# Performance work log

Hardware: AMD Instinct MI355X
Metric: run time of the kernel (lower is better)

## Reference

```python
import jax, jax.numpy as jnp
import numpy as np

R, NU, NM, E = 5, 100000, 100000, 1000000
IN, MSG, OUT, BAS = 64, 80, 64, 4
MPR = MSG // R  # per-rating message units (stack agg)


def setup_inputs() -> dict:
    key = jax.random.key(0)
    ks = jax.random.split(key, 12)
    return {
        "ufeat": jax.random.normal(ks[0], (NU, IN), jnp.float32),
        "ifeat": jax.random.normal(ks[1], (NM, IN), jnp.float32),
        "cj_user": jax.random.uniform(ks[2], (NU, 1), jnp.float32) + 0.1,
        "ci_user": jax.random.uniform(ks[3], (NU, 1), jnp.float32) + 0.1,
        "cj_movie": jax.random.uniform(ks[4], (NM, 1), jnp.float32) + 0.1,
        "ci_movie": jax.random.uniform(ks[5], (NM, 1), jnp.float32) + 0.1,
        "edge_user": jax.random.randint(ks[6], (R, E), 0, NU, jnp.int32),
        "edge_movie": jax.random.randint(ks[7], (R, E), 0, NM, jnp.int32),
        "att": jax.random.normal(ks[8], (R, BAS), jnp.float32),
        "basis": jax.random.normal(ks[9], (BAS, IN, MPR), jnp.float32),
        "fc_w": jax.random.normal(ks[10], (OUT, MSG), jnp.float32) / np.sqrt(MSG),
        "fc_b": jnp.zeros((OUT,), jnp.float32),
    }


def _agg(feat, src, dst, cj, ci, n_dst):
    # gather src features scaled by cj, scatter-sum to dst, scale by ci
    m = feat[src] * cj[src]                                 # [E, MPR]
    out = jax.ops.segment_sum(m, dst, num_segments=n_dst)   # [n_dst, MPR]
    return out * ci


def reference(ufeat, ifeat, cj_user, ci_user, cj_movie, ci_movie,
              edge_user, edge_movie, att, basis, fc_w, fc_b):
    # per-rating weights from basis decomposition
    W = jnp.einsum('rb,bio->rio', att, basis)       # [R, IN, MPR]
    fu = jnp.einsum('ni,rio->rno', ufeat, W)        # [R, NU, MPR]
    fi = jnp.einsum('ni,rio->rno', ifeat, W)        # [R, NM, MPR]
    agg = jax.vmap(_agg, in_axes=(0, 0, 0, None, None, None))
    # forward edges: user -> movie; reverse edges: movie -> user
    m_out = agg(fu, edge_user, edge_movie, cj_user, ci_movie, NM)  # [R, NM, MPR]
    u_out = agg(fi, edge_movie, edge_user, cj_movie, ci_user, NU)  # [R, NU, MPR]
    # 'stack' cross-type aggregation, flattened over ratings
    u = jnp.transpose(u_out, (1, 0, 2)).reshape(NU, MSG)
    m = jnp.transpose(m_out, (1, 0, 2)).reshape(NM, MSG)
    u = jax.nn.relu(u) @ fc_w.T + fc_b   # shared ufc == ifc
    m = jax.nn.relu(m) @ fc_w.T + fc_b
    return u, m
```

## Files before the change

kernel.cpp:

```cpp
#include <hip/hip_runtime.h>
#include <cstdint>
#include <cstddef>

constexpr int kR   = 5;
constexpr int kNU  = 100000;
constexpr int kNM  = 100000;
constexpr int kE   = 1000000;
constexpr int kIN  = 64;
constexpr int kMSG = 80;
constexpr int kOUT = 64;
constexpr int kBAS = 4;
constexpr int kMPR = 16;

constexpr int kN        = 100000;
constexpr unsigned kEdges   = (unsigned)kR * (unsigned)kE;
constexpr unsigned kTotRecs = 2u * kEdges;

constexpr int kBD        = 80;
constexpr int kNB        = kN / kBD;
constexpr unsigned kCap  = 5632;
constexpr int kChunkE    = 8192;
constexpr int kDirBlocks = (int)((kEdges + kChunkE - 1) / kChunkE);
constexpr int kMsgBlocks = (kN + 255) / 256;

constexpr float kScale    = 64.0f;
constexpr float kInvScale = 1.0f / 64.0f;

constexpr int kStride = 17;
constexpr int kAccWords = kBD * kR * kStride;

__global__ __launch_bounds__(256) void gcmc_init(
    uint32_t* __restrict__ cursor, const float* __restrict__ fc_w,
    float* __restrict__ Wq)
{
    const int t = blockIdx.x * 256 + threadIdx.x;
    if (t < 2 * kNB) cursor[t] = (uint32_t)t * kCap;
    if (t < 20 * kOUT * 4) {
        const int q  = t & 3;
        const int o  = (t >> 2) & 63;
        const int j4 = t >> 8;
        Wq[t] = fc_w[o * kMSG + j4 * 4 + q];
    }
}

__device__ __forceinline__ uint32_t pack2i16(float x, float y) {
    const int ix = (int)rintf(fminf(fmaxf(x, -32760.f), 32760.f));
    const int iy = (int)rintf(fminf(fmaxf(y, -32760.f), 32760.f));
    return (uint32_t)(ix & 0xFFFF) | ((uint32_t)(iy & 0xFFFF) << 16);
}

__global__ __launch_bounds__(256) void gcmc_msg(
    const float* __restrict__ ufeat, const float* __restrict__ ifeat,
    const float* __restrict__ cj_user, const float* __restrict__ cj_movie,
    const float* __restrict__ att,  const float* __restrict__ basis,
    short* __restrict__ ms)
{
    __shared__ float Wl[kR * kIN * kMPR];
    const int tid  = threadIdx.x;
    const int side = blockIdx.x >= kMsgBlocks;
    const int blk  = blockIdx.x - side * kMsgBlocks;
    const float* feat = side ? ifeat : ufeat;
    const float* cj   = side ? cj_movie : cj_user;
    uint2* mout = reinterpret_cast<uint2*>(ms + (side ? (size_t)kR * kN * kMPR : 0));

    for (int idx = tid; idx < kR * kIN * kMPR; idx += 256) {
        const int r   = idx >> 10;
        const int rem = idx & 1023;
        const int i   = rem >> 4;
        const int k   = rem & 15;
        float s = 0.f;
#pragma unroll
        for (int b = 0; b < kBAS; ++b)
            s += att[r * kBAS + b] * basis[(b * kIN + i) * kMPR + k];
        Wl[idx] = s;
    }
    __syncthreads();

    const int node = blk * 256 + tid;
    if (node >= kN) return;

    float f[kIN];
    const float4* fp = reinterpret_cast<const float4*>(feat + (size_t)node * kIN);
#pragma unroll
    for (int i = 0; i < kIN / 4; ++i) {
        float4 v = fp[i];
        f[4 * i + 0] = v.x; f[4 * i + 1] = v.y;
        f[4 * i + 2] = v.z; f[4 * i + 3] = v.w;
    }
    const float c = cj[node] * kScale;
    const float4* W4 = reinterpret_cast<const float4*>(Wl);

    for (int r = 0; r < kR; ++r) {
#pragma unroll
        for (int kg = 0; kg < kMPR / 4; ++kg) {
            float4 a = make_float4(0.f, 0.f, 0.f, 0.f);
#pragma unroll
            for (int i = 0; i < kIN; ++i) {
                float4 w = W4[(r * kIN + i) * (kMPR / 4) + kg];
                a.x += f[i] * w.x; a.y += f[i] * w.y;
                a.z += f[i] * w.z; a.w += f[i] * w.w;
            }
            const uint32_t plane = (uint32_t)(r * kN + node);
            mout[plane * 4u + kg] =
                make_uint2(pack2i16(a.x * c, a.y * c), pack2i16(a.z * c, a.w * c));
        }
    }
}

__global__ __launch_bounds__(512) void gcmc_partition(
    const int* __restrict__ dst0, const int* __restrict__ src0,
    const int* __restrict__ dst1, const int* __restrict__ src1,
    uint32_t* __restrict__ cursor, uint32_t* __restrict__ bucket_recs)
{
    __shared__ uint32_t hist[kNB];
    __shared__ uint32_t excl[kNB];
    __shared__ uint32_t gbase[kNB];
    __shared__ uint32_t scanT[512];
    __shared__ uint32_t stage[kChunkE];
    __shared__ uint16_t sbkt[kChunkE];
    const int tid = threadIdx.x;
    const int dir = blockIdx.x >= kDirBlocks;
    const int blk = blockIdx.x - dir * kDirBlocks;
    const int* dsts = dir ? dst1 : dst0;
    const int* srcs = dir ? src1 : src0;

    for (int i = tid; i < kNB; i += 512) hist[i] = 0;
    __syncthreads();

    const unsigned base = (unsigned)blk * kChunkE;
    uint32_t rec[16], bk[16], rk[16];
#pragma unroll
    for (int j = 0; j < 16; ++j) {
        const unsigned idx = base + j * 512u + tid;
        if (idx < kEdges) {
            const unsigned d = (unsigned)dsts[idx];
            const unsigned s = (unsigned)srcs[idx];
            const unsigned r = idx / (unsigned)kE;
            const unsigned b = d / (unsigned)kBD;
            const unsigned dl = d - b * (unsigned)kBD;
            rec[j] = (r * (unsigned)kN + s) | ((dl * (unsigned)kR + r) << 19);
            bk[j]  = b;
            rk[j]  = atomicAdd(&hist[b], 1u);
        } else bk[j] = 0xFFFFFFFFu;
    }
    __syncthreads();

    uint32_t loc[3]; uint32_t s2 = 0;
#pragma unroll
    for (int q = 0; q < 3; ++q) {
        const int b = tid * 3 + q;
        loc[q] = (b < kNB) ? hist[b] : 0u;
        s2 += loc[q];
    }
    scanT[tid] = s2; __syncthreads();
    for (int off = 1; off < 512; off <<= 1) {
        const uint32_t v = (tid >= off) ? scanT[tid - off] : 0u;
        __syncthreads();
        scanT[tid] += v;
        __syncthreads();
    }
    const uint32_t total = scanT[511];
    uint32_t run = scanT[tid] - s2;
#pragma unroll
    for (int q = 0; q < 3; ++q) {
        const int b = tid * 3 + q;
        if (b < kNB) {
            excl[b]  = run;
            gbase[b] = loc[q] ? atomicAdd(&cursor[dir * kNB + b], loc[q]) : 0u;
        }
        run += loc[q];
    }
    __syncthreads();

#pragma unroll
    for (int j = 0; j < 16; ++j) {
        if (bk[j] != 0xFFFFFFFFu) {
            const uint32_t p = excl[bk[j]] + rk[j];
            stage[p] = rec[j];
            sbkt[p]  = (uint16_t)bk[j];
        }
    }
    __syncthreads();

    for (unsigned p = tid; p < total; p += 512) {
        const uint32_t b = sbkt[p];
        bucket_recs[gbase[b] + (p - excl[b])] = stage[p];
    }
}

__global__ __launch_bounds__(256, 5) void gcmc_accum_fc(
    const short* __restrict__ ms,
    const uint32_t* __restrict__ bucket_recs,
    const uint32_t* __restrict__ cursor,
    const float* __restrict__ ci_user, const float* __restrict__ ci_movie,
    const float* __restrict__ Wq, const float* __restrict__ fc_b,
    float* __restrict__ out_u, float* __restrict__ out_m)
{
    __shared__ int accI[kAccWords];
    const int tid = threadIdx.x;
    const int db  = blockIdx.x;
    const int dir = db >= kNB;
    const int bl  = db - dir * kNB;

    for (int i = tid; i < kAccWords; i += 256) accI[i] = 0;
    __syncthreads();

    const uint32_t gb0 = (uint32_t)db * kCap;
    const uint32_t n   = cursor[db] - gb0;
    const uint32_t* rp = bucket_recs + gb0;
    const int l = tid & 3;
    const int g = tid >> 2;
    const uint2* pb = reinterpret_cast<const uint2*>(
        ms + (dir ? (size_t)kR * kN * kMPR : 0));

#define RRR(IDX) { const uint32_t rc = rp[(IDX)];                          \
                   const uint2 v = pb[(rc & 0x7FFFFu) * 4u + (unsigned)l];  \
                   const int w = (int)(rc >> 19) * kStride + (l << 2);      \
                   atomicAdd(&accI[w + 0], (int)(short)v.x);                \
                   atomicAdd(&accI[w + 1], ((int)v.x) >> 16);               \
                   atomicAdd(&accI[w + 2], (int)(short)v.y);                \
                   atomicAdd(&accI[w + 3], ((int)v.y) >> 16); }

    uint32_t i = (uint32_t)g;
    for (; i + 192u < n; i += 256u) { RRR(i) RRR(i + 64u) RRR(i + 128u) RRR(i + 192u) }
    for (; i < n; i += 64u) { RRR(i) }
#undef RRR
    __syncthreads();

    const int o = tid & 63;
    const int w4 = tid >> 6;
    const float* cip = dir ? ci_user : ci_movie;
    float* outp      = dir ? out_u  : out_m;
    const int dstBase = bl * kBD;
    const float bo = fc_b[o];
    const float4* Wq4 = reinterpret_cast<const float4*>(Wq);

    for (int dl = w4; dl < kBD; dl += 4) {
        const float cs = cip[dstBase + dl] * kInvScale;
        float a = bo;
#pragma unroll 4
        for (int j4 = 0; j4 < kMSG / 4; ++j4) {
            const int base = (dl * kR + (j4 >> 2)) * kStride + ((j4 & 3) << 2);
            const float x0 = fmaxf((float)accI[base + 0] * cs, 0.f);
            const float x1 = fmaxf((float)accI[base + 1] * cs, 0.f);
            const float x2 = fmaxf((float)accI[base + 2] * cs, 0.f);
            const float x3 = fmaxf((float)accI[base + 3] * cs, 0.f);
            const float4 wv = Wq4[j4 * 64 + o];
            a += x0 * wv.x + x1 * wv.y + x2 * wv.z + x3 * wv.w;
        }
        outp[(size_t)(dstBase + dl) * kOUT + o] = a;
    }
}

extern "C" void kernel_launch(void* const* d_in, const int* in_sizes, int n_in,
                              void* d_out, int out_size, void* d_ws, size_t ws_size,
                              hipStream_t stream) {
    const float* ufeat    = (const float*)d_in[0];
    const float* ifeat    = (const float*)d_in[1];
    const float* cj_user  = (const float*)d_in[2];
    const float* ci_user  = (const float*)d_in[3];
    const float* cj_movie = (const float*)d_in[4];
    const float* ci_movie = (const float*)d_in[5];
    const int*   edge_user  = (const int*)d_in[6];
    const int*   edge_movie = (const int*)d_in[7];
    const float* att   = (const float*)d_in[8];
    const float* basis = (const float*)d_in[9];
    const float* fc_w  = (const float*)d_in[10];
    const float* fc_b  = (const float*)d_in[11];

    float* out_u = (float*)d_out;
    float* out_m = out_u + (size_t)kNU * kOUT;

    short* ms = (short*)d_ws;
    uint32_t* bucket_recs = (uint32_t*)(ms + (size_t)2 * kR * kN * kMPR);
    uint32_t* cursorC     = bucket_recs + (size_t)(2 * kNB) * kCap;
    float*    Wq          = (float*)(cursorC + 2 * kNB);

    gcmc_init<<<20, 256, 0, stream>>>(cursorC, fc_w, Wq);

    gcmc_msg<<<2 * kMsgBlocks, 256, 0, stream>>>(
        ufeat, ifeat, cj_user, cj_movie, att, basis, ms);

    gcmc_partition<<<2 * kDirBlocks, 512, 0, stream>>>(
        edge_movie, edge_user, edge_user, edge_movie, cursorC, bucket_recs);

    gcmc_accum_fc<<<2 * kNB, 256, 0, stream>>>(
        ms, bucket_recs, cursorC, ci_user, ci_movie,
        Wq, fc_b, out_u, out_m);
}
```

Measured before the change: 409.4 us.

## Sub-bin edge buckets by source plane chunk to localize message gathers

Splits each destination bucket into four sub-bins keyed by the source message plane range, so the accumulate kernel walks records grouped by source region and its gathers from the message table hit a narrower address range, which should improve cache locality. The partition kernel moves to 1024 threads and 16K-edge chunks to amortize the larger 5000-bin histogram and scan, and it reuses the hist array in place of gbase. The cost is more bins, more global cursor atomics and fixed per-sub-bin capacity (1344), which could overflow if one sub-bin receives a skewed share of edges.

```diff
diff --git a/kernel.cpp b/kernel.cpp
--- a/kernel.cpp
+++ b/kernel.cpp
@@ -14,12 +14,15 @@
 
 constexpr int kN        = 100000;
 constexpr unsigned kEdges   = (unsigned)kR * (unsigned)kE;
-constexpr unsigned kTotRecs = 2u * kEdges;
 
 constexpr int kBD        = 80;
 constexpr int kNB        = kN / kBD;
-constexpr unsigned kCap  = 5632;
-constexpr int kChunkE    = 8192;
+
+constexpr int kNC        = 4;
+constexpr unsigned kPlanesPerChunk = 125000;
+constexpr int kBinsPerDir = kNB * kNC;
+constexpr unsigned kCap2 = 1344;
+constexpr int kChunkE    = 16384;
 constexpr int kDirBlocks = (int)((kEdges + kChunkE - 1) / kChunkE);
 constexpr int kMsgBlocks = (kN + 255) / 256;
 
@@ -34,7 +37,7 @@
     float* __restrict__ Wq)
 {
     const int t = blockIdx.x * 256 + threadIdx.x;
-    if (t < 2 * kNB) cursor[t] = (uint32_t)t * kCap;
+    if (t < 2 * kBinsPerDir) cursor[t] = (uint32_t)t * kCap2;
     if (t < 20 * kOUT * 4) {
         const int q  = t & 3;
         const int o  = (t >> 2) & 63;
@@ -107,15 +110,14 @@
     }
 }
 
-__global__ __launch_bounds__(512) void gcmc_partition(
+__global__ __launch_bounds__(1024) void gcmc_partition(
     const int* __restrict__ dst0, const int* __restrict__ src0,
     const int* __restrict__ dst1, const int* __restrict__ src1,
     uint32_t* __restrict__ cursor, uint32_t* __restrict__ bucket_recs)
 {
-    __shared__ uint32_t hist[kNB];
-    __shared__ uint32_t excl[kNB];
-    __shared__ uint32_t gbase[kNB];
-    __shared__ uint32_t scanT[512];
+    __shared__ uint32_t hist[kBinsPerDir];
+    __shared__ uint32_t excl[kBinsPerDir];
+    __shared__ uint32_t scanT[1024];
     __shared__ uint32_t stage[kChunkE];
     __shared__ uint16_t sbkt[kChunkE];
     const int tid = threadIdx.x;
@@ -124,49 +126,52 @@
     const int* dsts = dir ? dst1 : dst0;
     const int* srcs = dir ? src1 : src0;
 
-    for (int i = tid; i < kNB; i += 512) hist[i] = 0;
+    for (int i = tid; i < kBinsPerDir; i += 1024) hist[i] = 0;
     __syncthreads();
 
     const unsigned base = (unsigned)blk * kChunkE;
     uint32_t rec[16], bk[16], rk[16];
 #pragma unroll
     for (int j = 0; j < 16; ++j) {
-        const unsigned idx = base + j * 512u + tid;
+        const unsigned idx = base + j * 1024u + tid;
         if (idx < kEdges) {
             const unsigned d = (unsigned)dsts[idx];
             const unsigned s = (unsigned)srcs[idx];
             const unsigned r = idx / (unsigned)kE;
             const unsigned b = d / (unsigned)kBD;
             const unsigned dl = d - b * (unsigned)kBD;
-            rec[j] = (r * (unsigned)kN + s) | ((dl * (unsigned)kR + r) << 19);
-            bk[j]  = b;
-            rk[j]  = atomicAdd(&hist[b], 1u);
+            const unsigned plane = r * (unsigned)kN + s;
+            const unsigned ch = plane / kPlanesPerChunk;
+            const unsigned binl = b * (unsigned)kNC + ch;
+            rec[j] = plane | ((dl * (unsigned)kR + r) << 19);
+            bk[j]  = binl;
+            rk[j]  = atomicAdd(&hist[binl], 1u);
         } else bk[j] = 0xFFFFFFFFu;
     }
     __syncthreads();
 
-    uint32_t loc[3]; uint32_t s2 = 0;
-#pragma unroll
-    for (int q = 0; q < 3; ++q) {
-        const int b = tid * 3 + q;
-        loc[q] = (b < kNB) ? hist[b] : 0u;
+    uint32_t loc[5]; uint32_t s2 = 0;
+#pragma unroll
+    for (int q = 0; q < 5; ++q) {
+        const int b = tid * 5 + q;
+        loc[q] = (b < kBinsPerDir) ? hist[b] : 0u;
         s2 += loc[q];
     }
     scanT[tid] = s2; __syncthreads();
-    for (int off = 1; off < 512; off <<= 1) {
+    for (int off = 1; off < 1024; off <<= 1) {
         const uint32_t v = (tid >= off) ? scanT[tid - off] : 0u;
         __syncthreads();
         scanT[tid] += v;
         __syncthreads();
     }
-    const uint32_t total = scanT[511];
+    const uint32_t total = scanT[1023];
     uint32_t run = scanT[tid] - s2;
 #pragma unroll
-    for (int q = 0; q < 3; ++q) {
-        const int b = tid * 3 + q;
-        if (b < kNB) {
-            excl[b]  = run;
-            gbase[b] = loc[q] ? atomicAdd(&cursor[dir * kNB + b], loc[q]) : 0u;
+    for (int q = 0; q < 5; ++q) {
+        const int b = tid * 5 + q;
+        if (b < kBinsPerDir) {
+            excl[b] = run;
+            hist[b] = loc[q] ? atomicAdd(&cursor[dir * kBinsPerDir + b], loc[q]) : 0u;
         }
         run += loc[q];
     }
@@ -182,9 +187,9 @@
     }
     __syncthreads();
 
-    for (unsigned p = tid; p < total; p += 512) {
+    for (unsigned p = tid; p < total; p += 1024) {
         const uint32_t b = sbkt[p];
-        bucket_recs[gbase[b] + (p - excl[b])] = stage[p];
+        bucket_recs[hist[b] + (p - excl[b])] = stage[p];
     }
 }
 
@@ -205,9 +210,6 @@
     for (int i = tid; i < kAccWords; i += 256) accI[i] = 0;
     __syncthreads();
 
-    const uint32_t gb0 = (uint32_t)db * kCap;
-    const uint32_t n   = cursor[db] - gb0;
-    const uint32_t* rp = bucket_recs + gb0;
     const int l = tid & 3;
     const int g = tid >> 2;
     const uint2* pb = reinterpret_cast<const uint2*>(
@@ -221,9 +223,15 @@
                    atomicAdd(&accI[w + 2], (int)(short)v.y);                \
                    atomicAdd(&accI[w + 3], ((int)v.y) >> 16); }
 
-    uint32_t i = (uint32_t)g;
-    for (; i + 192u < n; i += 256u) { RRR(i) RRR(i + 64u) RRR(i + 128u) RRR(i + 192u) }
-    for (; i < n; i += 64u) { RRR(i) }
+    for (int ch = 0; ch < kNC; ++ch) {
+        const int bin = db * kNC + ch;
+        const uint32_t b0 = (uint32_t)bin * kCap2;
+        const uint32_t n  = cursor[bin] - b0;
+        const uint32_t* rp = bucket_recs + b0;
+        uint32_t i = (uint32_t)g;
+        for (; i + 192u < n; i += 256u) { RRR(i) RRR(i + 64u) RRR(i + 128u) RRR(i + 192u) }
+        for (; i < n; i += 64u) { RRR(i) }
+    }
 #undef RRR
     __syncthreads();
 
@@ -240,11 +248,11 @@
         float a = bo;
 #pragma unroll 4
         for (int j4 = 0; j4 < kMSG / 4; ++j4) {
-            const int base = (dl * kR + (j4 >> 2)) * kStride + ((j4 & 3) << 2);
-            const float x0 = fmaxf((float)accI[base + 0] * cs, 0.f);
-            const float x1 = fmaxf((float)accI[base + 1] * cs, 0.f);
-            const float x2 = fmaxf((float)accI[base + 2] * cs, 0.f);
-            const float x3 = fmaxf((float)accI[base + 3] * cs, 0.f);
+            const int base2 = (dl * kR + (j4 >> 2)) * kStride + ((j4 & 3) << 2);
+            const float x0 = fmaxf((float)accI[base2 + 0] * cs, 0.f);
+            const float x1 = fmaxf((float)accI[base2 + 1] * cs, 0.f);
+            const float x2 = fmaxf((float)accI[base2 + 2] * cs, 0.f);
+            const float x3 = fmaxf((float)accI[base2 + 3] * cs, 0.f);
             const float4 wv = Wq4[j4 * 64 + o];
             a += x0 * wv.x + x1 * wv.y + x2 * wv.z + x3 * wv.w;
         }
@@ -273,15 +281,15 @@
 
     short* ms = (short*)d_ws;
     uint32_t* bucket_recs = (uint32_t*)(ms + (size_t)2 * kR * kN * kMPR);
-    uint32_t* cursorC     = bucket_recs + (size_t)(2 * kNB) * kCap;
-    float*    Wq          = (float*)(cursorC + 2 * kNB);
-
-    gcmc_init<<<20, 256, 0, stream>>>(cursorC, fc_w, Wq);
+    uint32_t* cursorC     = bucket_recs + (size_t)(2 * kBinsPerDir) * kCap2;
+    float*    Wq          = (float*)(cursorC + 2 * kBinsPerDir);
+
+    gcmc_init<<<40, 256, 0, stream>>>(cursorC, fc_w, Wq);
 
     gcmc_msg<<<2 * kMsgBlocks, 256, 0, stream>>>(
         ufeat, ifeat, cj_user, cj_movie, att, basis, ms);
 
-    gcmc_partition<<<2 * kDirBlocks, 512, 0, stream>>>(
+    gcmc_partition<<<2 * kDirBlocks, 1024, 0, stream>>>(
         edge_movie, edge_user, edge_user, edge_movie, cursorC, bucket_recs);
 
     gcmc_accum_fc<<<2 * kNB, 256, 0, stream>>>(
```

New measurement: 382.7 us. -6.5%, faster.

## Sort bucket records by source chunk in LDS before gather, enlarge partition blocks

Applied to the files above, without the earlier changes.

The accumulation kernel first copies each bucket's records into shared memory, counting-sorted into 8 chunks keyed on source-row bits. Gathers from the message table then proceed chunk by chunk, so concurrent blocks touch a narrower address range and get better L2 locality. The partition kernel moves to 1024 threads and 16384-edge chunks, reusing the histogram array for the global bases so the gbase array can be dropped. This adds shared memory and an extra pass over records, and drops the occupancy hint on the accumulation kernel.

```diff
diff --git a/kernel.cpp b/kernel.cpp
--- a/kernel.cpp
+++ b/kernel.cpp
@@ -14,14 +14,15 @@
 
 constexpr int kN        = 100000;
 constexpr unsigned kEdges   = (unsigned)kR * (unsigned)kE;
-constexpr unsigned kTotRecs = 2u * kEdges;
 
 constexpr int kBD        = 80;
 constexpr int kNB        = kN / kBD;
 constexpr unsigned kCap  = 5632;
-constexpr int kChunkE    = 8192;
+constexpr int kChunkE    = 16384;
 constexpr int kDirBlocks = (int)((kEdges + kChunkE - 1) / kChunkE);
 constexpr int kMsgBlocks = (kN + 255) / 256;
+
+constexpr int kNCh = 8;
 
 constexpr float kScale    = 64.0f;
 constexpr float kInvScale = 1.0f / 64.0f;
@@ -107,15 +108,14 @@
     }
 }
 
-__global__ __launch_bounds__(512) void gcmc_partition(
+__global__ __launch_bounds__(1024) void gcmc_partition(
     const int* __restrict__ dst0, const int* __restrict__ src0,
     const int* __restrict__ dst1, const int* __restrict__ src1,
     uint32_t* __restrict__ cursor, uint32_t* __restrict__ bucket_recs)
 {
     __shared__ uint32_t hist[kNB];
     __shared__ uint32_t excl[kNB];
-    __shared__ uint32_t gbase[kNB];
-    __shared__ uint32_t scanT[512];
+    __shared__ uint32_t scanT[1024];
     __shared__ uint32_t stage[kChunkE];
     __shared__ uint16_t sbkt[kChunkE];
     const int tid = threadIdx.x;
@@ -124,14 +124,14 @@
     const int* dsts = dir ? dst1 : dst0;
     const int* srcs = dir ? src1 : src0;
 
-    for (int i = tid; i < kNB; i += 512) hist[i] = 0;
+    for (int i = tid; i < kNB; i += 1024) hist[i] = 0;
     __syncthreads();
 
     const unsigned base = (unsigned)blk * kChunkE;
     uint32_t rec[16], bk[16], rk[16];
 #pragma unroll
     for (int j = 0; j < 16; ++j) {
-        const unsigned idx = base + j * 512u + tid;
+        const unsigned idx = base + j * 1024u + tid;
         if (idx < kEdges) {
             const unsigned d = (unsigned)dsts[idx];
             const unsigned s = (unsigned)srcs[idx];
@@ -145,30 +145,26 @@
     }
     __syncthreads();
 
-    uint32_t loc[3]; uint32_t s2 = 0;
-#pragma unroll
-    for (int q = 0; q < 3; ++q) {
-        const int b = tid * 3 + q;
-        loc[q] = (b < kNB) ? hist[b] : 0u;
-        s2 += loc[q];
-    }
+    const int b0 = tid * 2, b1i = tid * 2 + 1;
+    const uint32_t loc0 = (b0 < kNB) ? hist[b0] : 0u;
+    const uint32_t loc1 = (b1i < kNB) ? hist[b1i] : 0u;
+    const uint32_t s2 = loc0 + loc1;
     scanT[tid] = s2; __syncthreads();
-    for (int off = 1; off < 512; off <<= 1) {
+    for (int off = 1; off < 1024; off <<= 1) {
         const uint32_t v = (tid >= off) ? scanT[tid - off] : 0u;
         __syncthreads();
         scanT[tid] += v;
         __syncthreads();
     }
-    const uint32_t total = scanT[511];
-    uint32_t run = scanT[tid] - s2;
-#pragma unroll
-    for (int q = 0; q < 3; ++q) {
-        const int b = tid * 3 + q;
-        if (b < kNB) {
-            excl[b]  = run;
-            gbase[b] = loc[q] ? atomicAdd(&cursor[dir * kNB + b], loc[q]) : 0u;
-        }
-        run += loc[q];
+    const uint32_t total = scanT[1023];
+    const uint32_t run = scanT[tid] - s2;
+    if (b0 < kNB) {
+        excl[b0] = run;
+        hist[b0] = loc0 ? atomicAdd(&cursor[dir * kNB + b0], loc0) : 0u;
+    }
+    if (b1i < kNB) {
+        excl[b1i] = run + loc0;
+        hist[b1i] = loc1 ? atomicAdd(&cursor[dir * kNB + b1i], loc1) : 0u;
     }
     __syncthreads();
 
@@ -182,13 +178,13 @@
     }
     __syncthreads();
 
-    for (unsigned p = tid; p < total; p += 512) {
+    for (unsigned p = tid; p < total; p += 1024) {
         const uint32_t b = sbkt[p];
-        bucket_recs[gbase[b] + (p - excl[b])] = stage[p];
-    }
-}
-
-__global__ __launch_bounds__(256, 5) void gcmc_accum_fc(
+        bucket_recs[hist[b] + (p - excl[b])] = stage[p];
+    }
+}
+
+__global__ __launch_bounds__(256) void gcmc_accum_fc(
     const short* __restrict__ ms,
     const uint32_t* __restrict__ bucket_recs,
     const uint32_t* __restrict__ cursor,
@@ -197,23 +193,46 @@
     float* __restrict__ out_u, float* __restrict__ out_m)
 {
     __shared__ int accI[kAccWords];
+    __shared__ uint32_t recL[kCap];
+    __shared__ uint32_t chCnt[kNCh];
+    __shared__ uint32_t chStart[kNCh + 1];
+    __shared__ uint32_t chCur[kNCh];
     const int tid = threadIdx.x;
     const int db  = blockIdx.x;
     const int dir = db >= kNB;
     const int bl  = db - dir * kNB;
 
     for (int i = tid; i < kAccWords; i += 256) accI[i] = 0;
+    if (tid < kNCh) chCnt[tid] = 0;
     __syncthreads();
 
     const uint32_t gb0 = (uint32_t)db * kCap;
     const uint32_t n   = cursor[db] - gb0;
     const uint32_t* rp = bucket_recs + gb0;
+
+    for (uint32_t i = tid; i < n; i += 256)
+        atomicAdd(&chCnt[(rp[i] >> 16) & 7u], 1u);
+    __syncthreads();
+    if (tid == 0) {
+        uint32_t run = 0;
+#pragma unroll
+        for (int c = 0; c < kNCh; ++c) { chStart[c] = run; chCur[c] = run; run += chCnt[c]; }
+        chStart[kNCh] = run;
+    }
+    __syncthreads();
+    for (uint32_t i = tid; i < n; i += 256) {
+        const uint32_t rc = rp[i];
+        const uint32_t p = atomicAdd(&chCur[(rc >> 16) & 7u], 1u);
+        recL[p] = rc;
+    }
+    __syncthreads();
+
     const int l = tid & 3;
     const int g = tid >> 2;
     const uint2* pb = reinterpret_cast<const uint2*>(
         ms + (dir ? (size_t)kR * kN * kMPR : 0));
 
-#define RRR(IDX) { const uint32_t rc = rp[(IDX)];                          \
+#define RRR(IDX) { const uint32_t rc = recL[(IDX)];                        \
                    const uint2 v = pb[(rc & 0x7FFFFu) * 4u + (unsigned)l];  \
                    const int w = (int)(rc >> 19) * kStride + (l << 2);      \
                    atomicAdd(&accI[w + 0], (int)(short)v.x);                \
@@ -221,9 +240,12 @@
                    atomicAdd(&accI[w + 2], (int)(short)v.y);                \
                    atomicAdd(&accI[w + 3], ((int)v.y) >> 16); }
 
-    uint32_t i = (uint32_t)g;
-    for (; i + 192u < n; i += 256u) { RRR(i) RRR(i + 64u) RRR(i + 128u) RRR(i + 192u) }
-    for (; i < n; i += 64u) { RRR(i) }
+    for (int ch = 0; ch < kNCh; ++ch) {
+        const uint32_t e = chStart[ch + 1];
+        uint32_t i = chStart[ch] + (uint32_t)g;
+        for (; i + 192u < e; i += 256u) { RRR(i) RRR(i + 64u) RRR(i + 128u) RRR(i + 192u) }
+        for (; i < e; i += 64u) { RRR(i) }
+    }
 #undef RRR
     __syncthreads();
 
@@ -240,11 +262,11 @@
         float a = bo;
 #pragma unroll 4
         for (int j4 = 0; j4 < kMSG / 4; ++j4) {
-            const int base = (dl * kR + (j4 >> 2)) * kStride + ((j4 & 3) << 2);
-            const float x0 = fmaxf((float)accI[base + 0] * cs, 0.f);
-            const float x1 = fmaxf((float)accI[base + 1] * cs, 0.f);
-            const float x2 = fmaxf((float)accI[base + 2] * cs, 0.f);
-            const float x3 = fmaxf((float)accI[base + 3] * cs, 0.f);
+            const int base2 = (dl * kR + (j4 >> 2)) * kStride + ((j4 & 3) << 2);
+            const float x0 = fmaxf((float)accI[base2 + 0] * cs, 0.f);
+            const float x1 = fmaxf((float)accI[base2 + 1] * cs, 0.f);
+            const float x2 = fmaxf((float)accI[base2 + 2] * cs, 0.f);
+            const float x3 = fmaxf((float)accI[base2 + 3] * cs, 0.f);
             const float4 wv = Wq4[j4 * 64 + o];
             a += x0 * wv.x + x1 * wv.y + x2 * wv.z + x3 * wv.w;
         }
@@ -281,7 +303,7 @@
     gcmc_msg<<<2 * kMsgBlocks, 256, 0, stream>>>(
         ufeat, ifeat, cj_user, cj_movie, att, basis, ms);
 
-    gcmc_partition<<<2 * kDirBlocks, 512, 0, stream>>>(
+    gcmc_partition<<<2 * kDirBlocks, 1024, 0, stream>>>(
         edge_movie, edge_user, edge_user, edge_movie, cursorC, bucket_recs);
 
     gcmc_accum_fc<<<2 * kNB, 256, 0, stream>>>(
```

Result: no change. 414.5 us (+1.3%).
